# Kernel optimization log

Hardware: AMD Instinct MI355X
Metric: run time of the kernel (lower is better)

The kernel has to match this reference:

```python
import jax, jax.numpy as jnp
import numpy as np

D_MODEL = 768
N_HEADS = 12
D_K = D_MODEL // N_HEADS
NEG_INF = -1e9


def setup_inputs() -> dict:
    key = jax.random.key(0)
    ks = jax.random.split(key, 7)
    B, S = 4, 2048
    x = jax.random.normal(ks[0], (B, S, D_MODEL), dtype=jnp.float32)
    # causal mask, broadcastable to [B, H, S, S]
    mask = jnp.tril(jnp.ones((S, S), dtype=bool))[None, None, :, :]
    scale = 1.0 / np.sqrt(D_MODEL)
    Wq = jax.random.normal(ks[1], (D_MODEL, D_MODEL), dtype=jnp.float32) * scale
    bq = jnp.zeros((D_MODEL,), dtype=jnp.float32)
    Wk = jax.random.normal(ks[2], (D_MODEL, D_MODEL), dtype=jnp.float32) * scale
    bk = jnp.zeros((D_MODEL,), dtype=jnp.float32)
    Wv = jax.random.normal(ks[3], (D_MODEL, D_MODEL), dtype=jnp.float32) * scale
    bv = jnp.zeros((D_MODEL,), dtype=jnp.float32)
    return {"x": x, "mask": mask, "Wq": Wq, "bq": bq, "Wk": Wk, "bk": bk, "Wv": Wv, "bv": bv}


def reference(x, mask, Wq, bq, Wk, bk, Wv, bv):
    B, S, _ = x.shape
    # projections (torch Linear: y = x @ W.T + b)
    q = (x @ Wq.T + bq).reshape(B, S, N_HEADS, D_K)
    k = (x @ Wk.T + bk).reshape(B, S, N_HEADS, D_K)
    v = (x @ Wv.T + bv).reshape(B, S, N_HEADS, D_K)
    # scores: [B, H, S, S]
    scores = jnp.einsum("bqhd,bkhd->bhqk", q, k) / jnp.sqrt(jnp.float32(D_K))
    scores = jnp.where(mask, scores, NEG_INF)
    probs = jax.nn.softmax(scores, axis=-1)
    # attention: [B, H, S, D_K] -> [B, S, d_model]
    attn = jnp.einsum("bhqk,bkhd->bqhd", probs, v).reshape(B, S, D_MODEL)
    return attn
```

## Files before the change

kernel.cpp:

```cpp
#include <hip/hip_runtime.h>
#include <math.h>


#define S_LEN 2048
#define BATCH 4
#define HEADS 12
#define DM 768
#define DK 64
#define BH (BATCH*HEADS)
#define MROWS (BATCH*S_LEN)
#define QSCALE 0.1803368801111244f

typedef __attribute__((ext_vector_type(8))) short short8;
typedef __attribute__((ext_vector_type(4))) float floatx4;
typedef __attribute__((ext_vector_type(16))) float floatx16;
typedef __attribute__((ext_vector_type(4))) unsigned int uintx4;
typedef __attribute__((address_space(3))) unsigned char lds_byte;
typedef __attribute__((address_space(1))) const unsigned char glob_byte;

__device__ __forceinline__ unsigned short f2bf(float f) {
  union { float f; unsigned int u; } a; a.f = f;
  unsigned int u = a.u;
  return (unsigned short)((u + 0x7fffu + ((u >> 16) & 1u)) >> 16);
}

__global__ __launch_bounds__(256) void cast_all(
    const float* __restrict__ x,
    const float* __restrict__ w0, const float* __restrict__ w1,
    const float* __restrict__ w2,
    unsigned short* __restrict__ xb, unsigned short* __restrict__ wb) {
  const int NX = MROWS * DM, NW = DM * DM;
  int i = (blockIdx.x * 256 + threadIdx.x) * 4;
  const float* src; unsigned short* dst; int off;
  if (i < NX) { src = x; dst = xb; off = i; }
  else {
    int kk = i - NX; int s = kk / NW; off = kk - s * NW;
    src = (s == 0) ? w0 : (s == 1) ? w1 : w2;
    dst = wb + (size_t)s * NW;
  }
  float4 v = *(const float4*)(src + off);
  ushort4 o;
  o.x = f2bf(v.x); o.y = f2bf(v.y); o.z = f2bf(v.z); o.w = f2bf(v.w);
  *(ushort4*)(dst + off) = o;
}

__global__ __launch_bounds__(256) void qkv_gemm(
    const unsigned short* __restrict__ xb,
    const unsigned short* __restrict__ wb,
    const float* __restrict__ bq, const float* __restrict__ bk,
    const float* __restrict__ bv,
    unsigned short* __restrict__ qo,
    unsigned short* __restrict__ ko,
    unsigned short* __restrict__ vto) {
  __shared__ unsigned short a_lds[2 * 128 * 32];
  __shared__ unsigned short b_lds[2 * 128 * 32];
  const int mat = blockIdx.z;
  const int tid = threadIdx.x;
  const int wave = tid >> 6, lane = tid & 63, quad = lane >> 4, ln = lane & 15;
  const int wm = wave & 1, wn = wave >> 1;
  const int m_blk = blockIdx.x * 128, n_blk = blockIdx.y * 128;
  const unsigned short* w = wb + (size_t)mat * DM * DM;
  const int srow_i[2] = { (0 * 256 + wave * 64 + lane) >> 2,
                          (1 * 256 + wave * 64 + lane) >> 2 };
  const int sq = (lane & 3) * 8;

  const floatx4 fz = {0.f, 0.f, 0.f, 0.f};
  floatx4 acc[4][4];
#pragma unroll
  for (int mg = 0; mg < 4; mg++)
#pragma unroll
    for (int c = 0; c < 4; c++) acc[mg][c] = fz;

  for (int k0 = 0; k0 < DM; k0 += 64) {
#pragma unroll
    for (int p = 0; p < 2; p++)
#pragma unroll
      for (int i = 0; i < 2; i++) {
        const int cbase = i * 256 + wave * 64;
        const int row = srow_i[i];
        __builtin_amdgcn_global_load_lds(
            (glob_byte*)(xb + (size_t)(m_blk + row) * DM + k0 + p * 32 + sq),
            (lds_byte*)(a_lds + p * 4096 + cbase * 8), 16, 0, 0);
        __builtin_amdgcn_global_load_lds(
            (glob_byte*)(w + (size_t)(n_blk + row) * DM + k0 + p * 32 + sq),
            (lds_byte*)(b_lds + p * 4096 + cbase * 8), 16, 0, 0);
      }
    __syncthreads();

    short8 af[4][2], bf[4][2];
#pragma unroll
    for (int mg = 0; mg < 4; mg++)
#pragma unroll
      for (int p = 0; p < 2; p++)
        af[mg][p] = *(const short8*)(a_lds + p * 4096 + (wm * 64 + mg * 16 + ln) * 32 + quad * 8);
#pragma unroll
    for (int c = 0; c < 4; c++)
#pragma unroll
      for (int p = 0; p < 2; p++)
        bf[c][p] = *(const short8*)(b_lds + p * 4096 + (wn * 64 + c * 16 + ln) * 32 + quad * 8);
#pragma unroll
    for (int mg = 0; mg < 4; mg++)
#pragma unroll
      for (int c = 0; c < 4; c++) {
        acc[mg][c] = __builtin_amdgcn_mfma_f32_16x16x32_bf16(af[mg][0], bf[c][0], acc[mg][c], 0, 0, 0);
        acc[mg][c] = __builtin_amdgcn_mfma_f32_16x16x32_bf16(af[mg][1], bf[c][1], acc[mg][c], 0, 0, 0);
      }
    __syncthreads();
  }

  const float* bias = (mat == 0) ? bq : (mat == 1) ? bk : bv;
  const float oscale = (mat == 0) ? QSCALE : 1.0f;
  const int m_base = m_blk + wm * 64, n_base = n_blk + wn * 64;
#pragma unroll
  for (int mg = 0; mg < 4; mg++)
#pragma unroll
    for (int c = 0; c < 4; c++) {
      int gn = n_base + c * 16 + ln;
      int hd = gn >> 6, d = gn & 63;
      float bias_v = bias[gn] * oscale;
      int gm0 = m_base + mg * 16 + quad * 4;
      int bb = gm0 >> 11, s0 = gm0 & (S_LEN - 1);
      if (mat == 2) {
        ushort4 pk;
        pk.x = f2bf(acc[mg][c][0] + bias_v);
        pk.y = f2bf(acc[mg][c][1] + bias_v);
        pk.z = f2bf(acc[mg][c][2] + bias_v);
        pk.w = f2bf(acc[mg][c][3] + bias_v);
        *(ushort4*)(vto + (((size_t)(bb * HEADS + hd)) * DK + d) * S_LEN + s0) = pk;
      } else {
        unsigned short* dst = (mat == 0 ? qo : ko) +
            (((size_t)(bb * HEADS + hd)) * S_LEN + s0) * DK + d;
#pragma unroll
        for (int r = 0; r < 4; r++)
          dst[(size_t)r * DK] = f2bf(acc[mg][c][r] * oscale + bias_v);
      }
    }
}

__global__ __launch_bounds__(256) void flash_attn(
    const unsigned short* __restrict__ q,
    const unsigned short* __restrict__ k,
    const unsigned short* __restrict__ vt,
    float* __restrict__ out) {
  __shared__ unsigned short k_lds[2][64 * 64];
  __shared__ unsigned short v_lds[2][64 * 64];
  const int id0 = blockIdx.x;
  const int rr = id0 >> 8, jj = id0 & 255;
  const int g = (rr == 0) ? jj : (rr == 1) ? (511 - jj) : (512 + jj);
  const int bh = g % BH;
  const int qt = (S_LEN / 128 - 1) - (g / BH);
  const int q0 = qt * 128;
  const int tid = threadIdx.x;
  const int wave = tid >> 6, lane = tid & 63;
  const int l31 = lane & 31, hi = lane >> 5;
  const unsigned short* qp = q + (size_t)bh * S_LEN * DK;
  const unsigned char* kpb = (const unsigned char*)(k  + (size_t)bh * S_LEN * DK);
  const unsigned char* vpb = (const unsigned char*)(vt + (size_t)bh * DK * S_LEN);
  const int qr_base = q0 + wave * 32;

  const floatx16 fz16 = {0.f,0.f,0.f,0.f,0.f,0.f,0.f,0.f,
                         0.f,0.f,0.f,0.f,0.f,0.f,0.f,0.f};

  short8 ones;
#pragma unroll
  for (int j = 0; j < 8; j++) ones[j] = (short)0x3F80;

  short8 aq[4];
#pragma unroll
  for (int ks = 0; ks < 4; ks++)
    aq[ks] = *(const short8*)(qp + (size_t)(qr_base + l31) * DK + ks * 16 + hi * 8);

  floatx16 o0 = fz16, o1 = fz16, lacc = fz16;

  const int sc0 = tid, sc1 = 256 + tid;
  const int sr[2]  = { sc0 >> 3, sc1 >> 3 };
  const int ssb[2] = { ((sc0 & 7) * 16) ^ ((sr[0] & 7) << 4),
                       ((sc1 & 7) * 16) ^ ((sr[1] & 7) << 4) };

  auto stage = [&](int nb, int k0) {
    unsigned short* kd = &k_lds[nb][0];
    unsigned short* vd = &v_lds[nb][0];
#pragma unroll
    for (int i = 0; i < 2; i++) {
      const int cbase = i * 256 + wave * 64;
      __builtin_amdgcn_global_load_lds(
          (glob_byte*)(kpb + (size_t)(k0 + sr[i]) * 128 + ssb[i]),
          (lds_byte*)(kd + cbase * 8), 16, 0, 0);
      __builtin_amdgcn_global_load_lds(
          (glob_byte*)(vpb + (size_t)sr[i] * (S_LEN * 2) + k0 * 2 + ssb[i]),
          (lds_byte*)(vd + cbase * 8), 16, 0, 0);
    }
  };

  const int xr = (l31 & 7) << 4;

  auto body = [&](int k0, int nb) {
    const unsigned char* kb = (const unsigned char*)&k_lds[nb][0];
    const unsigned char* vb = (const unsigned char*)&v_lds[nb][0];
    const bool domask = (k0 + 63 > qr_base);
#pragma unroll
    for (int kg = 0; kg < 2; kg++) {
      floatx16 sc = fz16;
#pragma unroll
      for (int ks = 0; ks < 4; ks++) {
        short8 kf = *(const short8*)(kb + (kg * 32 + l31) * 128 + ((ks * 32 + hi * 16) ^ xr));
        sc = __builtin_amdgcn_mfma_f32_32x32x16_bf16(kf, aq[ks], sc, 0, 0, 0);
      }
      float pv[16];
      const int qr = qr_base + l31;
#pragma unroll
      for (int r = 0; r < 16; r++) {
        float e = exp2f(sc[r]);
        if (domask) {
          int key = k0 + kg * 32 + (r & 3) + 8 * (r >> 2) + 4 * hi;
          e = (key <= qr) ? e : 0.f;
        }
        pv[r] = e;
      }
      unsigned int dw[4][2];
#pragma unroll
      for (int b = 0; b < 4; b++)
#pragma unroll
        for (int c = 0; c < 2; c++)
          asm("v_cvt_pk_bf16_f32 %0, %1, %2"
              : "=v"(dw[b][c]) : "v"(pv[4 * b + 2 * c]), "v"(pv[4 * b + 2 * c + 1]));
#pragma unroll
      for (int ks2 = 0; ks2 < 2; ks2++) {
        unsigned int a0 = dw[2 * ks2][0], a1 = dw[2 * ks2][1];
        unsigned int b0 = dw[2 * ks2 + 1][0], b1 = dw[2 * ks2 + 1][1];
        asm("v_permlane32_swap_b32 %0, %1" : "+v"(a0), "+v"(b0));
        asm("v_permlane32_swap_b32 %0, %1" : "+v"(a1), "+v"(b1));
        union { uintx4 u; short8 s; } ap;
        ap.u = (uintx4){a0, a1, b0, b1};
        short8 vf0 = *(const short8*)(vb + (0 * 32 + l31) * 128 + ((kg * 64 + ks2 * 32 + hi * 16) ^ xr));
        short8 vf1 = *(const short8*)(vb + (1 * 32 + l31) * 128 + ((kg * 64 + ks2 * 32 + hi * 16) ^ xr));
        o0 = __builtin_amdgcn_mfma_f32_32x32x16_bf16(ap.s, vf0, o0, 0, 0, 0);
        o1 = __builtin_amdgcn_mfma_f32_32x32x16_bf16(ap.s, vf1, o1, 0, 0, 0);
        lacc = __builtin_amdgcn_mfma_f32_32x32x16_bf16(ap.s, ones, lacc, 0, 0, 0);
      }
    }
  };

  const int nt = (q0 + 128) / 64;
  stage(0, 0);
  __syncthreads();
  int cur = 0;
#pragma unroll 1
  for (int t = 0; t < nt - 1; t++) {
    stage(cur ^ 1, (t + 1) * 64);
    if (t * 64 <= qr_base + 31) body(t * 64, cur);
    __syncthreads();
    cur ^= 1;
  }
  if ((nt - 1) * 64 <= qr_base + 31) body((nt - 1) * 64, cur);

  const int b = bh / HEADS, hd = bh % HEADS;
#pragma unroll
  for (int r = 0; r < 16; r++) {
    float inv = 1.f / lacc[r];
    int qrow = qr_base + (r & 3) + 8 * (r >> 2) + 4 * hi;
    float* orow = out + ((size_t)(b * S_LEN + qrow)) * DM + hd * DK;
    orow[l31]      = o0[r] * inv;
    orow[32 + l31] = o1[r] * inv;
  }
}

extern "C" void kernel_launch(void* const* d_in, const int* in_sizes, int n_in,
                              void* d_out, int out_size, void* d_ws, size_t ws_size,
                              hipStream_t stream) {
  const float* x  = (const float*)d_in[0];
  const float* Wq = (const float*)d_in[2];
  const float* bq = (const float*)d_in[3];
  const float* Wk = (const float*)d_in[4];
  const float* bk = (const float*)d_in[5];
  const float* Wv = (const float*)d_in[6];
  const float* bv = (const float*)d_in[7];
  float* out = (float*)d_out;

  const int NX = MROWS * DM;
  const int NW = DM * DM;
  const size_t NQK = (size_t)BH * S_LEN * DK;
  unsigned short* xb = (unsigned short*)d_ws;
  unsigned short* wb = xb + NX;
  unsigned short* qo = wb + 3 * NW;
  unsigned short* ko = qo + NQK;
  unsigned short* vt = ko + NQK;

  cast_all<<<(NX + 3 * NW) / 4 / 256, 256, 0, stream>>>(x, Wq, Wk, Wv, xb, wb);

  qkv_gemm<<<dim3(MROWS / 128, DM / 128, 3), 256, 0, stream>>>(
      xb, wb, bq, bk, bv, qo, ko, vt);

  flash_attn<<<dim3((S_LEN / 128) * BH), 256, 0, stream>>>(qo, ko, vt, out);
}
```

Before: 214.6 us.

## Split long causal query tiles across two blocks and combine partial outputs

Query tiles in the upper half of the sequence (qt 8-15) are each split into two blocks that cover disjoint key ranges. Each block writes unnormalized partial outputs and row sums, to the output buffer or to a workspace buffer. A new combine kernel adds the two partials and divides by the total sum. The aim is to even out work per block under the causal mask and shorten the critical path. The cost is an extra kernel launch and extra global traffic for the partials. There is no max subtraction, so summing raw partials stays consistent with the existing softmax.

```diff
diff --git a/kernel.cpp b/kernel.cpp
--- a/kernel.cpp
+++ b/kernel.cpp
@@ -141,15 +141,20 @@
     const unsigned short* __restrict__ q,
     const unsigned short* __restrict__ k,
     const unsigned short* __restrict__ vt,
-    float* __restrict__ out) {
+    float* __restrict__ out,
+    float* __restrict__ po1,
+    float* __restrict__ pl) {
   __shared__ unsigned short k_lds[2][64 * 64];
   __shared__ unsigned short v_lds[2][64 * 64];
-  const int id0 = blockIdx.x;
-  const int rr = id0 >> 8, jj = id0 & 255;
-  const int g = (rr == 0) ? jj : (rr == 1) ? (511 - jj) : (512 + jj);
-  const int bh = g % BH;
-  const int qt = (S_LEN / 128 - 1) - (g / BH);
+  const int id = blockIdx.x;
+  const int e = id / BH, bh = id % BH;
+  int qt, half, split;
+  if (e < 16) { qt = 15 - (e >> 1); half = e & 1; split = 1; }
+  else        { qt = 23 - e;        half = 0;     split = 0; }
   const int q0 = qt * 128;
+  const int nt_tot = 2 * qt + 2;
+  const int kbeg_t = (split && half) ? (qt + 1) : 0;
+  const int kend_t = (split && !half) ? (qt + 1) : nt_tot;
   const int tid = threadIdx.x;
   const int wave = tid >> 6, lane = tid & 63;
   const int l31 = lane & 31, hi = lane >> 5;
@@ -210,12 +215,12 @@
       const int qr = qr_base + l31;
 #pragma unroll
       for (int r = 0; r < 16; r++) {
-        float e = exp2f(sc[r]);
+        float e2 = exp2f(sc[r]);
         if (domask) {
           int key = k0 + kg * 32 + (r & 3) + 8 * (r >> 2) + 4 * hi;
-          e = (key <= qr) ? e : 0.f;
+          e2 = (key <= qr) ? e2 : 0.f;
         }
-        pv[r] = e;
+        pv[r] = e2;
       }
       unsigned int dw[4][2];
 #pragma unroll
@@ -241,28 +246,65 @@
     }
   };
 
-  const int nt = (q0 + 128) / 64;
-  stage(0, 0);
+  stage(0, kbeg_t * 64);
   __syncthreads();
   int cur = 0;
 #pragma unroll 1
-  for (int t = 0; t < nt - 1; t++) {
+  for (int t = kbeg_t; t < kend_t - 1; t++) {
     stage(cur ^ 1, (t + 1) * 64);
     if (t * 64 <= qr_base + 31) body(t * 64, cur);
     __syncthreads();
     cur ^= 1;
   }
-  if ((nt - 1) * 64 <= qr_base + 31) body((nt - 1) * 64, cur);
+  if ((kend_t - 1) * 64 <= qr_base + 31) body((kend_t - 1) * 64, cur);
 
   const int b = bh / HEADS, hd = bh % HEADS;
-#pragma unroll
-  for (int r = 0; r < 16; r++) {
-    float inv = 1.f / lacc[r];
-    int qrow = qr_base + (r & 3) + 8 * (r >> 2) + 4 * hi;
-    float* orow = out + ((size_t)(b * S_LEN + qrow)) * DM + hd * DK;
-    orow[l31]      = o0[r] * inv;
-    orow[32 + l31] = o1[r] * inv;
+  if (!split) {
+#pragma unroll
+    for (int r = 0; r < 16; r++) {
+      float inv = 1.f / lacc[r];
+      int qrow = qr_base + (r & 3) + 8 * (r >> 2) + 4 * hi;
+      float* orow = out + ((size_t)(b * S_LEN + qrow)) * DM + hd * DK;
+      orow[l31]      = o0[r] * inv;
+      orow[32 + l31] = o1[r] * inv;
+    }
+  } else {
+    float* obase = half ? po1 : out;
+    float* plh = pl + ((size_t)half * BH + bh) * S_LEN;
+#pragma unroll
+    for (int r = 0; r < 16; r++) {
+      int qrow = qr_base + (r & 3) + 8 * (r >> 2) + 4 * hi;
+      float* orow = obase + ((size_t)(b * S_LEN + qrow)) * DM + hd * DK;
+      orow[l31]      = o0[r];
+      orow[32 + l31] = o1[r];
+      if (l31 == 0) plh[qrow] = lacc[r];
+    }
   }
+}
+
+__global__ __launch_bounds__(256) void combine_out(
+    const float* __restrict__ po1,
+    const float* __restrict__ pl,
+    float* __restrict__ out) {
+  size_t gid = (size_t)blockIdx.x * 256 + threadIdx.x;
+  size_t idx = gid * 4;
+  int dm = (int)(idx % DM);
+  size_t rowg = idx / DM;
+  int b = (int)(rowg >> 10);
+  int s = (int)(S_LEN / 2 + (rowg & 1023));
+  int hd = dm >> 6;
+  size_t lidx = (size_t)(b * HEADS + hd) * S_LEN + s;
+  float l = pl[lidx] + pl[(size_t)BH * S_LEN + lidx];
+  float rl = 1.f / l;
+  size_t oi = ((size_t)(b * S_LEN + s)) * DM + dm;
+  float4 a = *(const float4*)(out + oi);
+  float4 c = *(const float4*)(po1 + oi);
+  float4 o;
+  o.x = (a.x + c.x) * rl;
+  o.y = (a.y + c.y) * rl;
+  o.z = (a.z + c.z) * rl;
+  o.w = (a.w + c.w) * rl;
+  *(float4*)(out + oi) = o;
 }
 
 extern "C" void kernel_launch(void* const* d_in, const int* in_sizes, int n_in,
@@ -285,11 +327,15 @@
   unsigned short* qo = wb + 3 * NW;
   unsigned short* ko = qo + NQK;
   unsigned short* vt = ko + NQK;
+  float* po1 = (float*)(vt + NQK);
+  float* pl  = po1 + (size_t)MROWS * DM;
 
   cast_all<<<(NX + 3 * NW) / 4 / 256, 256, 0, stream>>>(x, Wq, Wk, Wv, xb, wb);
 
   qkv_gemm<<<dim3(MROWS / 128, DM / 128, 3), 256, 0, stream>>>(
       xb, wb, bq, bk, bv, qo, ko, vt);
 
-  flash_attn<<<dim3((S_LEN / 128) * BH), 256, 0, stream>>>(qo, ko, vt, out);
-}
+  flash_attn<<<dim3(24 * BH), 256, 0, stream>>>(qo, ko, vt, out, po1, pl);
+
+  combine_out<<<(MROWS / 2 * DM / 4) / 256, 256, 0, stream>>>(po1, pl, out);
+}
```

Measured after the change: 221.1 us. +3.0%, slower.
